# Optimization experiments

Measured on AMD Instinct MI355X. Metric: run time of the kernel, lower is better.

The kernel has to match this reference:

```python
import jax, jax.numpy as jnp
import numpy as np


def setup_inputs() -> dict:
    key = jax.random.key(0)
    k1, k2 = jax.random.split(key)
    pred_m = jax.random.normal(k1, (64, 1, 512, 512), dtype=jnp.float32)
    # boxes: (x, y, s_x, s_y) per (batch, frame, target); values in [0, 256)
    multi_targets = jax.random.randint(k2, (64, 5, 32, 4), 0, 256, dtype=jnp.int32)
    return {"pred_m": pred_m, "multi_targets": multi_targets}


def _paint_heatmap(multi_targets, B, H, W, dtype):
    """Vectorized replacement for the triple-nested box-fill loop.

    Uses a 2D difference-array scatter + double cumsum: each box adds
    +1/-1 at its four corners; after prefix sums, count>0 marks painted
    pixels (original sets them to 255 regardless of overlap).
    """
    gt = multi_targets.reshape(B, -1, 4)  # [B, N, 4], N = n_frames*n_targets
    x, y, sx, sy = gt[..., 0], gt[..., 1], gt[..., 2], gt[..., 3]
    # python slicing clamps the end of the slice at H/W
    x1 = jnp.minimum(x, H)
    y1 = jnp.minimum(y, W)
    x2 = jnp.minimum(x + sx, H)
    y2 = jnp.minimum(y + sy, W)
    b_idx = jnp.broadcast_to(jnp.arange(B)[:, None], x.shape)
    diff = jnp.zeros((B, H + 1, W + 1), jnp.int32)
    diff = diff.at[b_idx, x1, y1].add(1)
    diff = diff.at[b_idx, x1, y2].add(-1)
    diff = diff.at[b_idx, x2, y1].add(-1)
    diff = diff.at[b_idx, x2, y2].add(1)
    count = jnp.cumsum(jnp.cumsum(diff, axis=1), axis=2)[:, :H, :W]
    return (count > 0).astype(dtype) * jnp.asarray(255.0, dtype)


def reference(pred_m, multi_targets):
    B, _, H, W = pred_m.shape
    heatmap = _paint_heatmap(multi_targets, B, H, W, pred_m.dtype)  # [B, H, W]
    target = heatmap[:, None]            # [B, 1, H, W]
    pred = jax.nn.sigmoid(pred_m)        # [B, 1, H, W]
    smooth = jnp.asarray(1.0, pred_m.dtype)
    intersection = jnp.sum(pred * target, axis=(1, 2, 3))
    pred_sum = jnp.sum(pred, axis=(1, 2, 3))
    target_sum = jnp.sum(target, axis=(1, 2, 3))
    loss = (intersection + smooth) / (pred_sum + target_sum - intersection + smooth)
    return 1.0 - jnp.mean(loss)
```

## Files before the change

### kernel.cpp

```cpp
#include <hip/hip_runtime.h>
#include <math.h>

#define SLICES 32
#define ROWS_PER_SLICE 16
#define NBOXES 160
#define THREADS 256

static __device__ __forceinline__ float fast_sigmoid(float x) {
    return __builtin_amdgcn_rcpf(1.0f + __expf(-x));
}

__global__ __launch_bounds__(THREADS, 8) void paint_reduce_kernel(
    const float* __restrict__ pred, const int* __restrict__ targets,
    float* __restrict__ partials)
{
    __shared__ unsigned s_mask[ROWS_PER_SLICE * 16];
    __shared__ float s_red[4 * 3];

    const int t = threadIdx.x;
    const int slice = blockIdx.x;
    const int b = blockIdx.y;
    const int r0 = slice * ROWS_PER_SLICE;
    const int lane = t & 63, wave = t >> 6;

    const int4* tg = (const int4*)targets + (size_t)b * NBOXES;
    int4 gb0 = tg[lane];
    int4 gb1 = tg[64 + lane];
    int4 gb2 = (lane < 32) ? tg[128 + lane] : make_int4(0, 0, 0, 0);

    unsigned px0, py0, px1, py1, px2, py2;
    auto clip = [&](int4 g, unsigned& px, unsigned& py) -> bool {
        int x1 = min(g.x, 512), y1 = min(g.y, 512);
        int x2 = min(g.x + g.z, 512), y2 = min(g.y + g.w, 512);
        int cx1 = max(x1, r0), cx2 = min(x2, r0 + ROWS_PER_SLICE);
        px = (unsigned)cx1 | ((unsigned)cx2 << 16);
        py = (unsigned)y1 | ((unsigned)y2 << 16);
        return (cx2 > cx1) && (y2 > y1);
    };
    bool k0 = clip(gb0, px0, py0);
    bool k1 = clip(gb1, px1, py1);
    bool k2 = clip(gb2, px2, py2) && (lane < 32);
    unsigned long long m0 = __ballot(k0);
    unsigned long long m1 = __ballot(k1);
    unsigned long long m2 = __ballot(k2);

    const float4* p4 = (const float4*)pred;
    const int col4 = t & 127;
    const int rb = t >> 7;
    const size_t gbase = (size_t)b * 65536 + (size_t)r0 * 128 + col4;
    float4 v0 = p4[gbase + (size_t)(rb + 0) * 128];
    float4 v1 = p4[gbase + (size_t)(rb + 2) * 128];
    float4 v2 = p4[gbase + (size_t)(rb + 4) * 128];
    float4 v3 = p4[gbase + (size_t)(rb + 6) * 128];
    __builtin_amdgcn_sched_barrier(0);

    const int r = r0 + (t >> 4);
    const unsigned wb = (unsigned)(t & 15) * 32u;
    unsigned m = 0;
    auto scan = [&](unsigned long long mk, unsigned px, unsigned py) {
        while (mk) {
            int k = (int)__builtin_ctzll(mk);
            mk &= mk - 1;
            unsigned rx = (unsigned)__builtin_amdgcn_readlane((int)px, k);
            unsigned ry = (unsigned)__builtin_amdgcn_readlane((int)py, k);
            int x1 = (int)(rx & 0xffffu), x2 = (int)(rx >> 16);
            unsigned y1 = ry & 0xffffu, y2 = ry >> 16;
            bool in_row = (r >= x1) && (r < x2);
            unsigned lo = y1 > wb ? y1 : wb;
            unsigned hi = y2 < wb + 32u ? y2 : wb + 32u;
            int nn = (int)hi - (int)lo;
            unsigned bits = 0xFFFFFFFFu >> ((32 - nn) & 31);
            unsigned contrib = bits << ((lo - wb) & 31u);
            m |= (in_row && nn > 0) ? contrib : 0u;
        }
    };
    scan(m0, px0, py0);
    scan(m1, px1, py1);
    scan(m2, px2, py2);
    s_mask[t] = m;
    __syncthreads();

    const int widx = col4 >> 3;
    const unsigned bb = (unsigned)(col4 & 7) * 4u;
    unsigned n0 = (s_mask[(rb +  0) * 16 + widx] >> bb) & 0xFu;
    unsigned n1 = (s_mask[(rb +  2) * 16 + widx] >> bb) & 0xFu;
    unsigned n2 = (s_mask[(rb +  4) * 16 + widx] >> bb) & 0xFu;
    unsigned n3 = (s_mask[(rb +  6) * 16 + widx] >> bb) & 0xFu;

    float4 v4 = p4[gbase + (size_t)(rb +  8) * 128];
    float4 v5 = p4[gbase + (size_t)(rb + 10) * 128];
    float4 v6 = p4[gbase + (size_t)(rb + 12) * 128];
    float4 v7 = p4[gbase + (size_t)(rb + 14) * 128];

    float psum = 0.0f, isum = 0.0f;
    int cnt = 0;
#define ACC(V, N)                                                       \
    {                                                                   \
        float s0 = fast_sigmoid((V).x);                                 \
        float s1 = fast_sigmoid((V).y);                                 \
        float s2 = fast_sigmoid((V).z);                                 \
        float s3 = fast_sigmoid((V).w);                                 \
        psum += (s0 + s1) + (s2 + s3);                                  \
        cnt += __popc(N);                                               \
        isum += (((N) & 1u) ? s0 : 0.0f) + (((N) & 2u) ? s1 : 0.0f)     \
              + (((N) & 4u) ? s2 : 0.0f) + (((N) & 8u) ? s3 : 0.0f);    \
    }
    ACC(v0, n0) ACC(v1, n1) ACC(v2, n2) ACC(v3, n3)

    unsigned n4 = (s_mask[(rb +  8) * 16 + widx] >> bb) & 0xFu;
    unsigned n5 = (s_mask[(rb + 10) * 16 + widx] >> bb) & 0xFu;
    unsigned n6 = (s_mask[(rb + 12) * 16 + widx] >> bb) & 0xFu;
    unsigned n7 = (s_mask[(rb + 14) * 16 + widx] >> bb) & 0xFu;
    ACC(v4, n4) ACC(v5, n5) ACC(v6, n6) ACC(v7, n7)
#undef ACC
    float csum = (float)cnt;

    for (int off = 32; off > 0; off >>= 1) {
        psum += __shfl_down(psum, off);
        isum += __shfl_down(isum, off);
        csum += __shfl_down(csum, off);
    }
    if (lane == 0) {
        s_red[wave * 3 + 0] = psum;
        s_red[wave * 3 + 1] = isum;
        s_red[wave * 3 + 2] = csum;
    }
    __syncthreads();
    if (t == 0) {
        float P = 0, I = 0, C = 0;
        for (int w = 0; w < 4; ++w) {
            P += s_red[w * 3 + 0];
            I += s_red[w * 3 + 1];
            C += s_red[w * 3 + 2];
        }
        float* o = partials + ((size_t)b * SLICES + slice) * 3;
        o[0] = P; o[1] = I; o[2] = C;
    }
}

__global__ __launch_bounds__(64) void final_kernel(
    const float* __restrict__ partials, float* __restrict__ out)
{
    const int b = threadIdx.x;
    double P = 0, I = 0, C = 0;
    for (int s = 0; s < SLICES; ++s) {
        const float* p = partials + ((size_t)b * SLICES + s) * 3;
        P += (double)p[0]; I += (double)p[1]; C += (double)p[2];
    }
    const double inter = 255.0 * I;
    const double tsum  = 255.0 * C;
    double loss = (inter + 1.0) / (P + tsum - inter + 1.0);
    for (int off = 32; off > 0; off >>= 1) loss += __shfl_down(loss, off);
    if (b == 0) out[0] = (float)(1.0 - loss / 64.0);
}

extern "C" void kernel_launch(void* const* d_in, const int* in_sizes, int n_in,
                              void* d_out, int out_size, void* d_ws, size_t ws_size,
                              hipStream_t stream) {
    const float* pred    = (const float*)d_in[0];
    const int*   targets = (const int*)d_in[1];
    float* out = (float*)d_out;
    float* partials = (float*)d_ws;

    dim3 grid(SLICES, 64);
    paint_reduce_kernel<<<grid, THREADS, 0, stream>>>(pred, targets, partials);
    final_kernel<<<1, 64, 0, stream>>>(partials, out);
}
```

Baseline: 106.7 us.

## Split mask painting into separate kernel and stream pred with global mask

Moves the box-to-bitmask painting into its own kernel, which writes a per-batch global bitmask. A second streaming kernel then loads all 8 pred float4s up front without shared memory or block barriers. Per-wave partials go straight to global, and the final kernel sums 128 entries per batch. The aim is to stop the box scan and syncthreads from stalling the memory stream, at the cost of an extra launch and a global mask round trip.

```diff
diff --git a/kernel.cpp b/kernel.cpp
--- a/kernel.cpp
+++ b/kernel.cpp
@@ -4,24 +4,19 @@
 #define SLICES 32
 #define ROWS_PER_SLICE 16
 #define NBOXES 160
-#define THREADS 256
 
 static __device__ __forceinline__ float fast_sigmoid(float x) {
     return __builtin_amdgcn_rcpf(1.0f + __expf(-x));
 }
 
-__global__ __launch_bounds__(THREADS, 8) void paint_reduce_kernel(
-    const float* __restrict__ pred, const int* __restrict__ targets,
-    float* __restrict__ partials)
+__global__ __launch_bounds__(256) void mask_kernel(
+    const int* __restrict__ targets, unsigned* __restrict__ gmask)
 {
-    __shared__ unsigned s_mask[ROWS_PER_SLICE * 16];
-    __shared__ float s_red[4 * 3];
-
     const int t = threadIdx.x;
     const int slice = blockIdx.x;
     const int b = blockIdx.y;
     const int r0 = slice * ROWS_PER_SLICE;
-    const int lane = t & 63, wave = t >> 6;
+    const int lane = t & 63;
 
     const int4* tg = (const int4*)targets + (size_t)b * NBOXES;
     int4 gb0 = tg[lane];
@@ -43,16 +38,6 @@
     unsigned long long m0 = __ballot(k0);
     unsigned long long m1 = __ballot(k1);
     unsigned long long m2 = __ballot(k2);
-
-    const float4* p4 = (const float4*)pred;
-    const int col4 = t & 127;
-    const int rb = t >> 7;
-    const size_t gbase = (size_t)b * 65536 + (size_t)r0 * 128 + col4;
-    float4 v0 = p4[gbase + (size_t)(rb + 0) * 128];
-    float4 v1 = p4[gbase + (size_t)(rb + 2) * 128];
-    float4 v2 = p4[gbase + (size_t)(rb + 4) * 128];
-    float4 v3 = p4[gbase + (size_t)(rb + 6) * 128];
-    __builtin_amdgcn_sched_barrier(0);
 
     const int r = r0 + (t >> 4);
     const unsigned wb = (unsigned)(t & 15) * 32u;
@@ -77,41 +62,60 @@
     scan(m0, px0, py0);
     scan(m1, px1, py1);
     scan(m2, px2, py2);
-    s_mask[t] = m;
-    __syncthreads();
+    gmask[(size_t)b * 8192 + (size_t)r0 * 16 + t] = m;
+}
 
+__global__ __launch_bounds__(256, 6) void stream_kernel(
+    const float* __restrict__ pred, const unsigned* __restrict__ gmask,
+    float* __restrict__ partials)
+{
+    const int t = threadIdx.x;
+    const int slice = blockIdx.x;
+    const int b = blockIdx.y;
+    const int r0 = slice * ROWS_PER_SLICE;
+    const int lane = t & 63, wave = t >> 6;
+    const int col4 = t & 127;
+    const int rb = t >> 7;
     const int widx = col4 >> 3;
     const unsigned bb = (unsigned)(col4 & 7) * 4u;
-    unsigned n0 = (s_mask[(rb +  0) * 16 + widx] >> bb) & 0xFu;
-    unsigned n1 = (s_mask[(rb +  2) * 16 + widx] >> bb) & 0xFu;
-    unsigned n2 = (s_mask[(rb +  4) * 16 + widx] >> bb) & 0xFu;
-    unsigned n3 = (s_mask[(rb +  6) * 16 + widx] >> bb) & 0xFu;
 
-    float4 v4 = p4[gbase + (size_t)(rb +  8) * 128];
-    float4 v5 = p4[gbase + (size_t)(rb + 10) * 128];
-    float4 v6 = p4[gbase + (size_t)(rb + 12) * 128];
-    float4 v7 = p4[gbase + (size_t)(rb + 14) * 128];
+    const unsigned* gm = gmask + (size_t)b * 8192 + (size_t)(r0 + rb) * 16 + widx;
+    unsigned w0 = gm[0 * 32];
+    unsigned w1 = gm[1 * 32];
+    unsigned w2 = gm[2 * 32];
+    unsigned w3 = gm[3 * 32];
+    unsigned w4 = gm[4 * 32];
+    unsigned w5 = gm[5 * 32];
+    unsigned w6 = gm[6 * 32];
+    unsigned w7 = gm[7 * 32];
+
+    const float4* p4 = (const float4*)pred;
+    const size_t g0 = (size_t)b * 65536 + (size_t)(r0 + rb) * 128 + col4;
+    float4 v0 = p4[g0 + 0 * 256];
+    float4 v1 = p4[g0 + 1 * 256];
+    float4 v2 = p4[g0 + 2 * 256];
+    float4 v3 = p4[g0 + 3 * 256];
+    float4 v4 = p4[g0 + 4 * 256];
+    float4 v5 = p4[g0 + 5 * 256];
+    float4 v6 = p4[g0 + 6 * 256];
+    float4 v7 = p4[g0 + 7 * 256];
 
     float psum = 0.0f, isum = 0.0f;
     int cnt = 0;
-#define ACC(V, N)                                                       \
+#define ACC(V, W)                                                       \
     {                                                                   \
+        const unsigned n = ((W) >> bb) & 0xFu;                          \
         float s0 = fast_sigmoid((V).x);                                 \
         float s1 = fast_sigmoid((V).y);                                 \
         float s2 = fast_sigmoid((V).z);                                 \
         float s3 = fast_sigmoid((V).w);                                 \
         psum += (s0 + s1) + (s2 + s3);                                  \
-        cnt += __popc(N);                                               \
-        isum += (((N) & 1u) ? s0 : 0.0f) + (((N) & 2u) ? s1 : 0.0f)     \
-              + (((N) & 4u) ? s2 : 0.0f) + (((N) & 8u) ? s3 : 0.0f);    \
+        cnt += __popc(n);                                               \
+        isum += ((n & 1u) ? s0 : 0.0f) + ((n & 2u) ? s1 : 0.0f)         \
+              + ((n & 4u) ? s2 : 0.0f) + ((n & 8u) ? s3 : 0.0f);        \
     }
-    ACC(v0, n0) ACC(v1, n1) ACC(v2, n2) ACC(v3, n3)
-
-    unsigned n4 = (s_mask[(rb +  8) * 16 + widx] >> bb) & 0xFu;
-    unsigned n5 = (s_mask[(rb + 10) * 16 + widx] >> bb) & 0xFu;
-    unsigned n6 = (s_mask[(rb + 12) * 16 + widx] >> bb) & 0xFu;
-    unsigned n7 = (s_mask[(rb + 14) * 16 + widx] >> bb) & 0xFu;
-    ACC(v4, n4) ACC(v5, n5) ACC(v6, n6) ACC(v7, n7)
+    ACC(v0, w0) ACC(v1, w1) ACC(v2, w2) ACC(v3, w3)
+    ACC(v4, w4) ACC(v5, w5) ACC(v6, w6) ACC(v7, w7)
 #undef ACC
     float csum = (float)cnt;
 
@@ -121,20 +125,8 @@
         csum += __shfl_down(csum, off);
     }
     if (lane == 0) {
-        s_red[wave * 3 + 0] = psum;
-        s_red[wave * 3 + 1] = isum;
-        s_red[wave * 3 + 2] = csum;
-    }
-    __syncthreads();
-    if (t == 0) {
-        float P = 0, I = 0, C = 0;
-        for (int w = 0; w < 4; ++w) {
-            P += s_red[w * 3 + 0];
-            I += s_red[w * 3 + 1];
-            C += s_red[w * 3 + 2];
-        }
-        float* o = partials + ((size_t)b * SLICES + slice) * 3;
-        o[0] = P; o[1] = I; o[2] = C;
+        float* o = partials + (((size_t)b * SLICES + slice) * 4 + wave) * 3;
+        o[0] = psum; o[1] = isum; o[2] = csum;
     }
 }
 
@@ -143,9 +135,11 @@
 {
     const int b = threadIdx.x;
     double P = 0, I = 0, C = 0;
-    for (int s = 0; s < SLICES; ++s) {
-        const float* p = partials + ((size_t)b * SLICES + s) * 3;
-        P += (double)p[0]; I += (double)p[1]; C += (double)p[2];
+    const float* p = partials + (size_t)b * SLICES * 4 * 3;
+    for (int s = 0; s < SLICES * 4; ++s) {
+        P += (double)p[s * 3 + 0];
+        I += (double)p[s * 3 + 1];
+        C += (double)p[s * 3 + 2];
     }
     const double inter = 255.0 * I;
     const double tsum  = 255.0 * C;
@@ -160,9 +154,12 @@
     const float* pred    = (const float*)d_in[0];
     const int*   targets = (const int*)d_in[1];
     float* out = (float*)d_out;
+
     float* partials = (float*)d_ws;
+    unsigned* gmask = (unsigned*)((char*)d_ws + (96 << 10));
 
     dim3 grid(SLICES, 64);
-    paint_reduce_kernel<<<grid, THREADS, 0, stream>>>(pred, targets, partials);
+    mask_kernel<<<grid, 256, 0, stream>>>(targets, gmask);
+    stream_kernel<<<grid, 256, 0, stream>>>(pred, gmask, partials);
     final_kernel<<<1, 64, 0, stream>>>(partials, out);
 }
```

Measured after the change: 118.7 us. 11.3% more time.
